# Kernel optimization log

Measured on AMD Instinct MI355X. Metric: run time of the kernel, lower is better.

## Reference

```python
import jax, jax.numpy as jnp
import numpy as np

N = 500_000
N_GROUPS = 50_000
D_IN = 64
D_OUT = 64
IN_MLP = D_IN * 3  # x, x - min, x - max (use_num=False)
NEG_SLOPE = 0.2


def setup_inputs() -> dict:
    key = jax.random.key(0)
    k_x, k_c, k_w1, k_w2 = jax.random.split(key, 4)
    x = jax.random.normal(k_x, (N, D_IN), dtype=jnp.float32)
    # CSR pointer: 0 = p0 <= p1 <= ... <= p_{n_groups} = N
    inner = jnp.sort(jax.random.randint(k_c, (N_GROUPS - 1,), 0, N))
    csr_idx = jnp.concatenate([jnp.zeros((1,), jnp.int64 if jax.config.jax_enable_x64 else jnp.int32),
                               inner.astype(jnp.int32),
                               jnp.full((1,), N, jnp.int32)]).astype(jnp.int32)
    # MLP([in_mlp, d_out, d_out], bias=False): two bias-free Linear layers,
    # each followed by LeakyReLU(0.2) (BatchNorm omitted / identity).
    w1 = jax.random.normal(k_w1, (IN_MLP, D_OUT), dtype=jnp.float32) / np.sqrt(IN_MLP)
    w2 = jax.random.normal(k_w2, (D_OUT, D_OUT), dtype=jnp.float32) / np.sqrt(D_OUT)
    return {"x": x, "csr_idx": csr_idx, "w1": w1, "w2": w2}


def _forward(x, csr_idx, w1, w2):
    n = x.shape[0]
    # element -> segment id (jit-safe equivalent of repeat_interleave on lengths)
    seg = jnp.searchsorted(csr_idx, jnp.arange(n, dtype=csr_idx.dtype), side='right') - 1  # [N]
    # segment min/max + gather-back
    seg_min = jax.ops.segment_min(x, seg, num_segments=N_GROUPS)  # [G, D]
    seg_max = jax.ops.segment_max(x, seg, num_segments=N_GROUPS)  # [G, D]
    x_map_min = x - seg_min[seg]
    x_map_max = x - seg_max[seg]
    h = jnp.concatenate([x, x_map_min, x_map_max], axis=1)  # [N, 3*D_IN]
    h = jax.nn.leaky_relu(h @ w1, NEG_SLOPE)
    h = jax.nn.leaky_relu(h @ w2, NEG_SLOPE)
    return h


def reference(x, csr_idx, w1, w2):
    return _forward(x, csr_idx, w1, w2)
```

## Files before the change

### kernel.cpp

```cpp
#include <hip/hip_runtime.h>
#include <math.h>

#define NROWS 500000
#define NGRP  50000
#define NEG   0.2f
#define GPB   16

typedef __attribute__((ext_vector_type(8))) short bf16x8;
typedef __attribute__((ext_vector_type(4))) float f32x4;
typedef unsigned int uint32;

__device__ __forceinline__ float leaky(float h) { return h >= 0.f ? h : NEG * h; }
__device__ __forceinline__ unsigned short f2bf(float v) {
    uint32 u = __float_as_uint(v);
    u += 0x7FFFu + ((u >> 16) & 1u);
    return (unsigned short)(u >> 16);
}
__device__ __forceinline__ float bf2f(unsigned short h) {
    return __uint_as_float((uint32)h << 16);
}

__global__ void k0_frag(const float* __restrict__ w1, const float* __restrict__ w2,
                        unsigned short* __restrict__ wsf, unsigned short* __restrict__ w2f,
                        unsigned short* __restrict__ wbh, unsigned short* __restrict__ wbl) {
    int r = blockIdx.x * 256 + threadIdx.x;
    if (r >= 8192) return;
    int j = r & 7, q = (r >> 3) & 3, n = (r >> 5) & 63;
    int k = (r >> 11) * 32 + q * 8 + j;
    if (r < 4096) {
        float ws = w1[k * 64 + n] + w1[4096 + k * 64 + n] + w1[8192 + k * 64 + n];
        wsf[r] = f2bf(ws);
        w2f[r] = f2bf(w2[k * 64 + n]);
    }
    float v = w1[(64 + k) * 64 + n];
    unsigned short h = f2bf(v);
    wbh[r] = h;
    wbl[r] = f2bf(v - bf2f(h));
}

__global__ __launch_bounds__(256, 6)
void fused(const float* __restrict__ x, const int* __restrict__ csr,
           const unsigned short* __restrict__ wsf,
           const unsigned short* __restrict__ w2f,
           const unsigned short* __restrict__ wbh,
           const unsigned short* __restrict__ wbl,
           float* __restrict__ out) {
    __shared__ __align__(16) short xb[64 * 72];
    __shared__ __align__(16) short y1s[64 * 72];
    __shared__ float biasL[GPB * 65];
    __shared__ __align__(16) int rowgrpL[64];
    __shared__ int csrl[GPB + 1];

    const int tid = threadIdx.x, w = tid >> 6, lane = tid & 63;
    const int q = lane >> 4, nl = lane & 15;
    const int jb = w * 16;
    const int n = jb + nl;

    const int g0 = blockIdx.x * GPB;
    const int ng = min(GPB, NGRP - g0);
    if (tid <= ng) csrl[tid] = csr[g0 + tid];
    __syncthreads();
    const int p0 = csrl[0], p1 = csrl[ng];

    float* mnF = (float*)y1s;
    {
        const int sub = q;
        const float4* xr = (const float4*)x;
        for (int gl = w; gl < ng; gl += 4) {
            int q0 = csrl[gl], cnt = csrl[gl + 1] - q0;
            if (cnt <= 0) continue;
            float4 mn = { INFINITY, INFINITY, INFINITY, INFINITY };
            float4 mx = { -INFINITY, -INFINITY, -INFINITY, -INFINITY };
            for (int i = 0; i < cnt; i += 16) {
                int ra = q0 + min(i + sub,      cnt - 1);
                int rb = q0 + min(i + sub + 4,  cnt - 1);
                int rc = q0 + min(i + sub + 8,  cnt - 1);
                int rd = q0 + min(i + sub + 12, cnt - 1);
                float4 a = xr[ra * 16 + nl], b = xr[rb * 16 + nl];
                float4 c = xr[rc * 16 + nl], d = xr[rd * 16 + nl];
                mn.x = fminf(mn.x, fminf(fminf(a.x, b.x), fminf(c.x, d.x)));
                mn.y = fminf(mn.y, fminf(fminf(a.y, b.y), fminf(c.y, d.y)));
                mn.z = fminf(mn.z, fminf(fminf(a.z, b.z), fminf(c.z, d.z)));
                mn.w = fminf(mn.w, fminf(fminf(a.w, b.w), fminf(c.w, d.w)));
                mx.x = fmaxf(mx.x, fmaxf(fmaxf(a.x, b.x), fmaxf(c.x, d.x)));
                mx.y = fmaxf(mx.y, fmaxf(fmaxf(a.y, b.y), fmaxf(c.y, d.y)));
                mx.z = fmaxf(mx.z, fmaxf(fmaxf(a.z, b.z), fmaxf(c.z, d.z)));
                mx.w = fmaxf(mx.w, fmaxf(fmaxf(a.w, b.w), fmaxf(c.w, d.w)));
            }
#pragma unroll
            for (int mk = 16; mk <= 32; mk <<= 1) {
                mn.x = fminf(mn.x, __shfl_xor(mn.x, mk));
                mn.y = fminf(mn.y, __shfl_xor(mn.y, mk));
                mn.z = fminf(mn.z, __shfl_xor(mn.z, mk));
                mn.w = fminf(mn.w, __shfl_xor(mn.w, mk));
                mx.x = fmaxf(mx.x, __shfl_xor(mx.x, mk));
                mx.y = fmaxf(mx.y, __shfl_xor(mx.y, mk));
                mx.z = fmaxf(mx.z, __shfl_xor(mx.z, mk));
                mx.w = fmaxf(mx.w, __shfl_xor(mx.w, mk));
            }
            if (sub == 0) {
                *(float4*)&mnF[gl * 132 + nl * 4]      = mn;
                *(float4*)&mnF[gl * 132 + 64 + nl * 4] = mx;
            }
        }
    }
    __syncthreads();

    {
        const bf16x8* bhv = (const bf16x8*)wbh;
        const bf16x8* blv = (const bf16x8*)wbl;
        f32x4 acc = { 0.f, 0.f, 0.f, 0.f };
#pragma unroll
        for (int ks = 0; ks < 4; ++ks) {
            bf16x8 Bh = bhv[(ks * 64 + n) * 4 + q];
            bf16x8 Bl = blv[(ks * 64 + n) * 4 + q];
            const float* ap = &mnF[nl * 132 + ks * 32 + q * 8];
            f32x4 v0 = *(const f32x4*)ap;
            f32x4 v1 = *(const f32x4*)(ap + 4);
            bf16x8 ah, al;
#pragma unroll
            for (int jj = 0; jj < 4; ++jj) {
                unsigned short h0 = f2bf(v0[jj]);
                unsigned short h1 = f2bf(v1[jj]);
                ah[jj]     = (short)h0;
                ah[4 + jj] = (short)h1;
                al[jj]     = (short)f2bf(v0[jj] - bf2f(h0));
                al[4 + jj] = (short)f2bf(v1[jj] - bf2f(h1));
            }
            acc = __builtin_amdgcn_mfma_f32_16x16x32_bf16(ah, Bh, acc, 0, 0, 0);
            acc = __builtin_amdgcn_mfma_f32_16x16x32_bf16(al, Bh, acc, 0, 0, 0);
            acc = __builtin_amdgcn_mfma_f32_16x16x32_bf16(ah, Bl, acc, 0, 0, 0);
        }
#pragma unroll
        for (int r = 0; r < 4; ++r)
            biasL[(q * 4 + r) * 65 + n] = -acc[r];
    }

    const bf16x8* wsv = (const bf16x8*)wsf;
    const bf16x8* w2v = (const bf16x8*)w2f;
    bf16x8 B0 = wsv[n * 4 + q];
    bf16x8 B1 = wsv[(64 + n) * 4 + q];
    bf16x8 C0 = w2v[n * 4 + q];
    bf16x8 C1 = w2v[(64 + n) * 4 + q];

    const int nch = (p1 - p0 + 63) >> 6;
    float4 stg[4];
    {
        int availf = min(64, p1 - p0) * 64;
        const float4* x4 = (const float4*)(x + (size_t)p0 * 64);
#pragma unroll
        for (int i = 0; i < 4; ++i) {
            int f = (i * 256 + tid) * 4;
            if (f < availf) stg[i] = x4[f >> 2];
        }
    }
    __syncthreads();

    for (int ch = 0; ch < nch; ++ch) {
        const int r0c  = p0 + (ch << 6);
        const int rows = min(64, p1 - r0c);
        const int availf = rows * 64;

#pragma unroll
        for (int i = 0; i < 4; ++i) {
            int f = (i * 256 + tid) * 4;
            if (f < availf) {
                float4 v = stg[i];
                int r = f >> 6, c = f & 63;
                uint32 lo = (uint32)f2bf(v.x) | ((uint32)f2bf(v.y) << 16);
                uint32 hi = (uint32)f2bf(v.z) | ((uint32)f2bf(v.w) << 16);
                *(uint32*)(&xb[r * 72 + c])     = lo;
                *(uint32*)(&xb[r * 72 + c + 2]) = hi;
            }
        }
        if (tid < 64) {
            int rs = min(r0c + tid, p1 - 1);
            int lo = 0, hi = ng;
#pragma unroll
            for (int it = 0; it < 5; ++it) {
                int mid = (lo + hi) >> 1;
                bool cb = csrl[mid] <= rs;
                lo = cb ? mid : lo;
                hi = cb ? hi : mid;
            }
            rowgrpL[tid] = lo;
        }
        __syncthreads();

        if (ch + 1 < nch) {
            int r0n = r0c + 64;
            int availn = min(64, p1 - r0n) * 64;
            const float4* x4 = (const float4*)(x + (size_t)r0n * 64);
#pragma unroll
            for (int i = 0; i < 4; ++i) {
                int f = (i * 256 + tid) * 4;
                if (f < availn) stg[i] = x4[f >> 2];
            }
        }

        f32x4 h[4];
#pragma unroll
        for (int mt = 0; mt < 4; ++mt) {
            int rbase = mt * 16 + q * 4;
            int4 grp = *(const int4*)(&rowgrpL[rbase]);
            f32x4 acc;
            acc.x = biasL[grp.x * 65 + n];
            acc.y = biasL[grp.y * 65 + n];
            acc.z = biasL[grp.z * 65 + n];
            acc.w = biasL[grp.w * 65 + n];
            bf16x8 a0 = *(const bf16x8*)(&xb[(mt * 16 + nl) * 72 + q * 8]);
            bf16x8 a1 = *(const bf16x8*)(&xb[(mt * 16 + nl) * 72 + 32 + q * 8]);
            acc = __builtin_amdgcn_mfma_f32_16x16x32_bf16(a0, B0, acc, 0, 0, 0);
            acc = __builtin_amdgcn_mfma_f32_16x16x32_bf16(a1, B1, acc, 0, 0, 0);
            h[mt] = acc;
        }
#pragma unroll
        for (int mt = 0; mt < 4; ++mt) {
            int rbase = mt * 16 + q * 4;
#pragma unroll
            for (int r = 0; r < 4; ++r)
                y1s[(rbase + r) * 72 + n] = (short)f2bf(leaky(h[mt][r]));
        }
        __syncthreads();

#pragma unroll
        for (int mt = 0; mt < 4; ++mt) {
            f32x4 acc = {0.f, 0.f, 0.f, 0.f};
            bf16x8 a0 = *(const bf16x8*)(&y1s[(mt * 16 + nl) * 72 + q * 8]);
            bf16x8 a1 = *(const bf16x8*)(&y1s[(mt * 16 + nl) * 72 + 32 + q * 8]);
            acc = __builtin_amdgcn_mfma_f32_16x16x32_bf16(a0, C0, acc, 0, 0, 0);
            acc = __builtin_amdgcn_mfma_f32_16x16x32_bf16(a1, C1, acc, 0, 0, 0);
            int rbase = mt * 16 + q * 4;
#pragma unroll
            for (int r = 0; r < 4; ++r) {
                int rl = rbase + r;
                if (rl < rows)
                    __builtin_nontemporal_store(leaky(acc[r]),
                        &out[(size_t)(r0c + rl) * 64 + n]);
            }
        }
    }
}

extern "C" void kernel_launch(void* const* d_in, const int* in_sizes, int n_in,
                              void* d_out, int out_size, void* d_ws, size_t ws_size,
                              hipStream_t stream) {
    const float* x   = (const float*)d_in[0];
    const int*   csr = (const int*)d_in[1];
    const float* w1  = (const float*)d_in[2];
    const float* w2  = (const float*)d_in[3];
    float* out = (float*)d_out;

    unsigned short* wsf = (unsigned short*)d_ws;
    unsigned short* w2f = wsf + 4096;
    unsigned short* wbh = wsf + 8192;
    unsigned short* wbl = wsf + 16384;

    k0_frag<<<32, 256, 0, stream>>>(w1, w2, wsf, w2f, wbh, wbl);
    const int grid = (NGRP + GPB - 1) / GPB;
    fused<<<grid, 256, 0, stream>>>(x, csr, wsf, w2f, wbh, wbl, out);
}
```

Measured before the change: 263.0 us.

## Use packed bf16 conversion, prefetch group min/max loads, and simplify leaky/store

Replaces software float-to-bf16 rounding with the hardware v_cvt_pk_bf16_f32 instruction in the weight-split, x staging and hidden-layer paths, cutting ALU work. It restructures the per-group min/max reduction so the first 16 rows of two groups are loaded up front, raising memory-level parallelism. LeakyReLU becomes fmaxf(h, 0.2h), and the output store drops the nontemporal hint. Several unrelated micro-optimizations are bundled, and removing the nontemporal hint may affect cache behaviour for the large output stream.

New measurement: 258.1 us. About the same (-1.9%).

```diff
diff --git a/kernel.cpp b/kernel.cpp
--- a/kernel.cpp
+++ b/kernel.cpp
@@ -10,7 +10,7 @@
 typedef __attribute__((ext_vector_type(4))) float f32x4;
 typedef unsigned int uint32;
 
-__device__ __forceinline__ float leaky(float h) { return h >= 0.f ? h : NEG * h; }
+__device__ __forceinline__ float leaky(float h) { return fmaxf(h, NEG * h); }
 __device__ __forceinline__ unsigned short f2bf(float v) {
     uint32 u = __float_as_uint(v);
     u += 0x7FFFu + ((u >> 16) & 1u);
@@ -18,6 +18,11 @@
 }
 __device__ __forceinline__ float bf2f(unsigned short h) {
     return __uint_as_float((uint32)h << 16);
+}
+__device__ __forceinline__ uint32 pkbf(float a, float b) {
+    uint32 r;
+    asm("v_cvt_pk_bf16_f32 %0, %1, %2" : "=v"(r) : "v"(a), "v"(b));
+    return r;
 }
 
 __global__ void k0_frag(const float* __restrict__ w1, const float* __restrict__ w2,
@@ -66,12 +71,20 @@
     {
         const int sub = q;
         const float4* xr = (const float4*)x;
-        for (int gl = w; gl < ng; gl += 4) {
-            int q0 = csrl[gl], cnt = csrl[gl + 1] - q0;
-            if (cnt <= 0) continue;
-            float4 mn = { INFINITY, INFINITY, INFINITY, INFINITY };
-            float4 mx = { -INFINITY, -INFINITY, -INFINITY, -INFINITY };
-            for (int i = 0; i < cnt; i += 16) {
+
+        auto redgrp = [&](int gl, int q0, int cnt,
+                          float4 r0, float4 r1, float4 r2, float4 r3) {
+            if (cnt <= 0) return;
+            float4 mn, mx;
+            mn.x = fminf(fminf(r0.x, r1.x), fminf(r2.x, r3.x));
+            mn.y = fminf(fminf(r0.y, r1.y), fminf(r2.y, r3.y));
+            mn.z = fminf(fminf(r0.z, r1.z), fminf(r2.z, r3.z));
+            mn.w = fminf(fminf(r0.w, r1.w), fminf(r2.w, r3.w));
+            mx.x = fmaxf(fmaxf(r0.x, r1.x), fmaxf(r2.x, r3.x));
+            mx.y = fmaxf(fmaxf(r0.y, r1.y), fmaxf(r2.y, r3.y));
+            mx.z = fmaxf(fmaxf(r0.z, r1.z), fmaxf(r2.z, r3.z));
+            mx.w = fmaxf(fmaxf(r0.w, r1.w), fmaxf(r2.w, r3.w));
+            for (int i = 16; i < cnt; i += 16) {
                 int ra = q0 + min(i + sub,      cnt - 1);
                 int rb = q0 + min(i + sub + 4,  cnt - 1);
                 int rc = q0 + min(i + sub + 8,  cnt - 1);
@@ -102,6 +115,25 @@
                 *(float4*)&mnF[gl * 132 + nl * 4]      = mn;
                 *(float4*)&mnF[gl * 132 + 64 + nl * 4] = mx;
             }
+        };
+
+#pragma unroll
+        for (int pr = 0; pr < 2; ++pr) {
+            const int gA = w + pr * 8, gB = gA + 4;
+            int qA = csrl[gA], cA = csrl[gA + 1] - qA;
+            int qB = csrl[gB], cB = csrl[gB + 1] - qB;
+            const int bA = (cA > 0) ? qA : 0, iA = max(cA - 1, 0);
+            const int bB = (cB > 0) ? qB : 0, iB = max(cB - 1, 0);
+            float4 a0 = xr[(bA + min(sub,      iA)) * 16 + nl];
+            float4 a1 = xr[(bA + min(sub + 4,  iA)) * 16 + nl];
+            float4 a2 = xr[(bA + min(sub + 8,  iA)) * 16 + nl];
+            float4 a3 = xr[(bA + min(sub + 12, iA)) * 16 + nl];
+            float4 b0 = xr[(bB + min(sub,      iB)) * 16 + nl];
+            float4 b1 = xr[(bB + min(sub + 4,  iB)) * 16 + nl];
+            float4 b2 = xr[(bB + min(sub + 8,  iB)) * 16 + nl];
+            float4 b3 = xr[(bB + min(sub + 12, iB)) * 16 + nl];
+            redgrp(gA, qA, cA, a0, a1, a2, a3);
+            redgrp(gB, qB, cB, b0, b1, b2, b3);
         }
     }
     __syncthreads();
@@ -117,19 +149,26 @@
             const float* ap = &mnF[nl * 132 + ks * 32 + q * 8];
             f32x4 v0 = *(const f32x4*)ap;
             f32x4 v1 = *(const f32x4*)(ap + 4);
-            bf16x8 ah, al;
-#pragma unroll
-            for (int jj = 0; jj < 4; ++jj) {
-                unsigned short h0 = f2bf(v0[jj]);
-                unsigned short h1 = f2bf(v1[jj]);
-                ah[jj]     = (short)h0;
-                ah[4 + jj] = (short)h1;
-                al[jj]     = (short)f2bf(v0[jj] - bf2f(h0));
-                al[4 + jj] = (short)f2bf(v1[jj] - bf2f(h1));
-            }
-            acc = __builtin_amdgcn_mfma_f32_16x16x32_bf16(ah, Bh, acc, 0, 0, 0);
-            acc = __builtin_amdgcn_mfma_f32_16x16x32_bf16(al, Bh, acc, 0, 0, 0);
-            acc = __builtin_amdgcn_mfma_f32_16x16x32_bf16(ah, Bl, acc, 0, 0, 0);
+            union U { bf16x8 v; uint32 u[4]; } ah, al;
+            ah.u[0] = pkbf(v0[0], v0[1]);
+            ah.u[1] = pkbf(v0[2], v0[3]);
+            ah.u[2] = pkbf(v1[0], v1[1]);
+            ah.u[3] = pkbf(v1[2], v1[3]);
+            float r0 = v0[0] - __uint_as_float(ah.u[0] << 16);
+            float r1 = v0[1] - __uint_as_float(ah.u[0] & 0xffff0000u);
+            float r2 = v0[2] - __uint_as_float(ah.u[1] << 16);
+            float r3 = v0[3] - __uint_as_float(ah.u[1] & 0xffff0000u);
+            float r4 = v1[0] - __uint_as_float(ah.u[2] << 16);
+            float r5 = v1[1] - __uint_as_float(ah.u[2] & 0xffff0000u);
+            float r6 = v1[2] - __uint_as_float(ah.u[3] << 16);
+            float r7 = v1[3] - __uint_as_float(ah.u[3] & 0xffff0000u);
+            al.u[0] = pkbf(r0, r1);
+            al.u[1] = pkbf(r2, r3);
+            al.u[2] = pkbf(r4, r5);
+            al.u[3] = pkbf(r6, r7);
+            acc = __builtin_amdgcn_mfma_f32_16x16x32_bf16(ah.v, Bh, acc, 0, 0, 0);
+            acc = __builtin_amdgcn_mfma_f32_16x16x32_bf16(al.v, Bh, acc, 0, 0, 0);
+            acc = __builtin_amdgcn_mfma_f32_16x16x32_bf16(ah.v, Bl, acc, 0, 0, 0);
         }
 #pragma unroll
         for (int r = 0; r < 4; ++r)
@@ -167,10 +206,10 @@
             if (f < availf) {
                 float4 v = stg[i];
                 int r = f >> 6, c = f & 63;
-                uint32 lo = (uint32)f2bf(v.x) | ((uint32)f2bf(v.y) << 16);
-                uint32 hi = (uint32)f2bf(v.z) | ((uint32)f2bf(v.w) << 16);
-                *(uint32*)(&xb[r * 72 + c])     = lo;
-                *(uint32*)(&xb[r * 72 + c + 2]) = hi;
+                uint2 p;
+                p.x = pkbf(v.x, v.y);
+                p.y = pkbf(v.z, v.w);
+                *(uint2*)(&xb[r * 72 + c]) = p;
             }
         }
         if (tid < 64) {
@@ -217,9 +256,16 @@
 #pragma unroll
         for (int mt = 0; mt < 4; ++mt) {
             int rbase = mt * 16 + q * 4;
-#pragma unroll
-            for (int r = 0; r < 4; ++r)
-                y1s[(rbase + r) * 72 + n] = (short)f2bf(leaky(h[mt][r]));
+            float h0 = leaky(h[mt][0]);
+            float h1 = leaky(h[mt][1]);
+            float h2 = leaky(h[mt][2]);
+            float h3 = leaky(h[mt][3]);
+            uint32 p01 = pkbf(h0, h1);
+            uint32 p23 = pkbf(h2, h3);
+            y1s[(rbase + 0) * 72 + n] = (short)(p01 & 0xffffu);
+            y1s[(rbase + 1) * 72 + n] = (short)(p01 >> 16);
+            y1s[(rbase + 2) * 72 + n] = (short)(p23 & 0xffffu);
+            y1s[(rbase + 3) * 72 + n] = (short)(p23 >> 16);
         }
         __syncthreads();
 
@@ -235,8 +281,7 @@
             for (int r = 0; r < 4; ++r) {
                 int rl = rbase + r;
                 if (rl < rows)
-                    __builtin_nontemporal_store(leaky(acc[r]),
-                        &out[(size_t)(r0c + rl) * 64 + n]);
+                    out[(size_t)(r0c + rl) * 64 + n] = leaky(acc[r]);
             }
         }
     }
```
